# Optimization experiments

Hardware: AMD Instinct MI355X
Metric: run time of the kernel (lower is better)

Reference implementation:

```python
import jax, jax.numpy as jnp
import numpy as np

N, DIN, D, K0, NC = 32768, 768, 512, 128, 2
KS = [128, 64, 32, 16]  # prototype counts per stage (num_protos // 2**i)
NEG_SLOPE = 0.01


def _lin(x, W, b):
    # torch nn.Linear: W is [out, in]
    return x @ W.T + b


def _ln(x, g, b):
    m = x.mean(-1, keepdims=True)
    v = ((x - m) ** 2).mean(-1, keepdims=True)
    return (x - m) * jax.lax.rsqrt(v + 1e-5) * g + b


def setup_inputs() -> dict:
    key = jax.random.key(0)
    ks = jax.random.split(key, 40)
    s = 0.02

    def nrm(k, shp, sc=s):
        return jax.random.normal(k, shp, jnp.float32) * sc

    inp = {}
    inp["data"] = jax.random.normal(ks[0], (N, DIN), jnp.float32)
    inp["prototypes"] = jax.random.normal(ks[1], (K0, DIN), jnp.float32)
    inp["W_pp"] = nrm(ks[2], (D, DIN)); inp["b_pp"] = jnp.zeros((D,), jnp.float32)
    inp["W_cp"] = nrm(ks[3], (D, DIN)); inp["b_cp"] = jnp.zeros((D,), jnp.float32)
    inp["sim_scale"] = jnp.ones((1,), jnp.float32)
    # 3 enhancer MLPs + layernorms (stacked, same shapes)
    inp["enh_w1"] = nrm(ks[4], (3, D, D)); inp["enh_b1"] = jnp.zeros((3, D), jnp.float32)
    inp["enh_w2"] = nrm(ks[5], (3, D, D)); inp["enh_b2"] = jnp.zeros((3, D), jnp.float32)
    inp["ln_g"] = jnp.ones((3, D), jnp.float32); inp["ln_b"] = jnp.zeros((3, D), jnp.float32)
    # ProtoReducers: Mlp along K axis; fc1 [inK,inK], fc2 [outK,inK]
    ki = 6
    for i in range(3):
        inK, outK = KS[i], KS[i + 1]
        inp[f"red_w1_{i}"] = nrm(ks[ki], (inK, inK)); ki += 1
        inp[f"red_b1_{i}"] = jnp.zeros((inK,), jnp.float32)
        inp[f"red_w2_{i}"] = nrm(ks[ki], (outK, inK)); ki += 1
        inp[f"red_b2_{i}"] = jnp.zeros((outK,), jnp.float32)
    inp["W_proc"] = nrm(ks[20], (D, D)); inp["b_proc"] = jnp.zeros((D,), jnp.float32)
    inp["g_an"] = jnp.ones((D,), jnp.float32); inp["b_an"] = jnp.zeros((D,), jnp.float32)
    inp["W_t"] = nrm(ks[21], (D, D)); inp["b_t"] = jnp.zeros((D,), jnp.float32)
    inp["W_g"] = nrm(ks[22], (D, D)); inp["b_g"] = jnp.zeros((D,), jnp.float32)
    inp["W_s"] = nrm(ks[23], (1, D)); inp["b_s"] = jnp.zeros((1,), jnp.float32)
    inp["W_h"] = nrm(ks[24], (D, D)); inp["b_h"] = jnp.zeros((D,), jnp.float32)
    inp["W_c"] = nrm(ks[25], (NC, D)); inp["b_c"] = jnp.zeros((NC,), jnp.float32)
    return inp


def reference(data, prototypes, W_pp, b_pp, W_cp, b_cp, sim_scale,
              enh_w1, enh_b1, enh_w2, enh_b2, ln_g, ln_b,
              red_w1_0, red_b1_0, red_w2_0, red_b2_0,
              red_w1_1, red_b1_1, red_w2_1, red_b2_1,
              red_w1_2, red_b1_2, red_w2_2, red_b2_2,
              W_proc, b_proc, g_an, b_an,
              W_t, b_t, W_g, b_g, W_s, b_s, W_h, b_h, W_c, b_c):
    # patch / prototype projections (Linear + LeakyReLU)
    P = jax.nn.leaky_relu(_lin(data, W_pp, b_pp), NEG_SLOPE)        # [N, D]
    C = jax.nn.leaky_relu(_lin(prototypes, W_cp, b_cp), NEG_SLOPE)  # [K0, D]
    # denom = max(1e-6, tau * similarity_scale.item()); tau=1, no grad through scale
    denom = jnp.maximum(1e-6, jax.lax.stop_gradient(sim_scale)[0])
    reds = [(red_w1_0, red_b1_0, red_w2_0, red_b2_0),
            (red_w1_1, red_b1_1, red_w2_1, red_b2_1),
            (red_w1_2, red_b1_2, red_w2_2, red_b2_2)]
    for i in range(3):
        # L2 similarity: -cdist(P, C) computed as a GEMM
        d2 = (jnp.sum(P * P, -1, keepdims=True) + jnp.sum(C * C, -1)[None, :]
              - 2.0 * (P @ C.T))
        sim = -jnp.sqrt(jnp.maximum(d2, 1e-12))                     # [N, K]
        A = jax.nn.softmax(sim / denom, axis=1)                     # soft routing
        ctx = A @ C                                                 # [N, D]
        P = _ln(P + ctx, ln_g[i], ln_b[i])
        P = P + _lin(jax.nn.relu(_lin(P, enh_w1[i], enh_b1[i])), enh_w2[i], enh_b2[i])
        # ProtoReducer: Mlp over K axis (operate on C.T of shape [D, K])
        w1, b1, w2, b2 = reds[i]
        Ct = _lin(jax.nn.relu(_lin(C.T, w1, b1)), w2, b2)           # [D, Kout]
        C = Ct.T
    Z = jnp.concatenate([P, C], axis=0)                             # [N+16, D]
    Z = jax.nn.relu(_lin(Z, W_proc, b_proc))
    Z = _ln(Z, g_an, b_an)
    # gated attention MIL pooling
    t = jnp.tanh(_lin(Z, W_t, b_t))
    g = jax.nn.sigmoid(_lin(Z, W_g, b_g))
    scores = _lin(t * g, W_s, b_s)                                  # [N+16, 1]
    Aw = jax.nn.softmax(scores, axis=0)
    bag = Aw.T @ Z                                                  # [1, D]
    h = jax.nn.relu(_lin(bag, W_h, b_h))
    logits = _lin(h, W_c, b_c)                                      # [1, 2]
    return logits
```

## Files before the change

kernel.cpp:

```cpp
#include <hip/hip_runtime.h>
#include <math.h>

typedef _Float16 f16x8 __attribute__((ext_vector_type(8)));
typedef _Float16 f16x4 __attribute__((ext_vector_type(4)));
typedef float f32x4 __attribute__((ext_vector_type(4)));

#define TBM 256
#define TBN 128
#define TBK 32

#define AS1 __attribute__((address_space(1)))
#define AS3 __attribute__((address_space(3)))

__device__ __forceinline__ void gll16(const _Float16* g, _Float16* l)
{
    __builtin_amdgcn_global_load_lds((const AS1 unsigned int*)g,
                                     (AS3 unsigned int*)l, 16, 0, 0);
}

__device__ __forceinline__ int xcd_swz(int d, int nwg)
{
    int q = nwg >> 3, r = nwg & 7;
    int x = d & 7, idx = d >> 3;
    int base = x < r ? x * (q + 1) : r * (q + 1) + (x - r) * q;
    return base + idx;
}

__device__ __forceinline__ float fsigmoid(float x)
{
    return __builtin_amdgcn_rcpf(1.f + __expf(-x));
}
__device__ __forceinline__ float ftanh(float x)
{
    float ax = fabsf(x);
    float e = __expf(-2.f * ax);
    float t = (1.f - e) * __builtin_amdgcn_rcpf(1.f + e);
    return copysignf(t, x);
}

template<int ACT, bool F16OUT>
__global__ __launch_bounds__(256)
void dot_k(const float* __restrict__ X, const float* __restrict__ W,
           const float* __restrict__ bias, void* __restrict__ Yv,
           int M, int K)
{
    int gw = (blockIdx.x * 256 + threadIdx.x) >> 6;
    int lane = threadIdx.x & 63;
    if (gw >= M * 512) return;
    int r = gw >> 9, n = gw & 511;
    const float* xr = X + (size_t)r * K;
    const float* wr = W + (size_t)n * K;
    float d = 0.f;
    for (int t = 0; t < K; t += 256) {
        float4 a = *(const float4*)(xr + t + lane * 4);
        float4 b = *(const float4*)(wr + t + lane * 4);
        d += a.x * b.x + a.y * b.y + a.z * b.z + a.w * b.w;
    }
#pragma unroll
    for (int o = 32; o; o >>= 1) d += __shfl_xor(d, o);
    if (lane == 0) {
        float v = d + bias[n];
        if (ACT == 1) v = v > 0.f ? v : 0.01f * v;
        else if (ACT == 2) v = fmaxf(v, 0.f);
        if (F16OUT) ((_Float16*)Yv)[(size_t)r * 512 + n] = (_Float16)v;
        else        ((float*)Yv)[(size_t)r * 512 + n] = v;
    }
}

__global__ __launch_bounds__(256)
void cvtC2_k(const float* __restrict__ C, _Float16* __restrict__ Ch,
             _Float16* __restrict__ CTh, float* __restrict__ Csq, int Kin)
{
    int w = threadIdx.x >> 6, lane = threadIdx.x & 63;
    int row = blockIdx.x * 4 + w;
    if (row >= Kin) return;
    float4 a = *(const float4*)(C + (size_t)row * 512 + lane * 8);
    float4 b = *(const float4*)(C + (size_t)row * 512 + lane * 8 + 4);
    f16x8 h;
    h[0] = (_Float16)a.x; h[1] = (_Float16)a.y; h[2] = (_Float16)a.z; h[3] = (_Float16)a.w;
    h[4] = (_Float16)b.x; h[5] = (_Float16)b.y; h[6] = (_Float16)b.z; h[7] = (_Float16)b.w;
    *(f16x8*)(Ch + (size_t)row * 512 + lane * 8) = h;
    float s = 0.f;
#pragma unroll
    for (int q = 0; q < 8; q++) {
        float f = (float)h[q];
        s += f * f;
        CTh[(size_t)(lane * 8 + q) * Kin + row] = h[q];
    }
#pragma unroll
    for (int o = 32; o; o >>= 1) s += __shfl_xor(s, o);
    if (lane == 0) Csq[row] = s;
}

template<int MODE, int ACT, bool SQ>
__global__ __launch_bounds__(512)
void mgemm(const _Float16* __restrict__ A, const _Float16* __restrict__ B,
           const float* __restrict__ bias, _Float16* __restrict__ Yh,
           float* __restrict__ Psq, int M, int K, int Nout)
{
    __shared__ _Float16 As[2][TBM * TBK];
    __shared__ _Float16 Bs[2][TBN * TBK];
    const int tid = threadIdx.x;
    const int lane = tid & 63;
    const int wid = tid >> 6;
    const int wr = wid >> 1, wc = wid & 1;

    int bid = xcd_swz(blockIdx.y * gridDim.x + blockIdx.x, gridDim.x * gridDim.y);
    const int m0 = (bid / gridDim.x) * TBM;
    const int n0 = (bid % gridDim.x) * TBN;

    f32x4 acc[4][4] = {};
    const int nt = K / TBK;

    const int lrow = lane >> 2;
    const int lk = (lane & 3) * 8;

    auto stage = [&](int t, int buf) {
        const int k0 = t * TBK;
#pragma unroll
        for (int q = 0; q < 2; q++) {
            int c = wid * 2 + q;
            int r = c * 16 + lrow;
            int am = min(m0 + r, M - 1);
            gll16(A + (size_t)am * K + k0 + lk, &As[buf][c * 512]);
        }
        {
            int c = wid;
            int r = c * 16 + lrow;
            int bn = min(n0 + r, Nout - 1);
            gll16(B + (size_t)bn * K + k0 + lk, &Bs[buf][c * 512]);
        }
    };

    stage(0, 0);
    __syncthreads();
    for (int t = 0; t < nt; ++t) {
        const int cur = t & 1;
        if (t + 1 < nt) stage(t + 1, cur ^ 1);
        f16x8 af[4], bf[4];
#pragma unroll
        for (int mi = 0; mi < 4; mi++)
            af[mi] = *(const f16x8*)(&As[cur][(wr * 64 + mi * 16 + (lane & 15)) * TBK + (lane >> 4) * 8]);
#pragma unroll
        for (int nj = 0; nj < 4; nj++)
            bf[nj] = *(const f16x8*)(&Bs[cur][(wc * 64 + nj * 16 + (lane & 15)) * TBK + (lane >> 4) * 8]);
#pragma unroll
        for (int mi = 0; mi < 4; mi++)
#pragma unroll
            for (int nj = 0; nj < 4; nj++)
                acc[mi][nj] = __builtin_amdgcn_mfma_f32_16x16x32_f16(af[mi], bf[nj], acc[mi][nj], 0, 0, 0);
        __syncthreads();
    }

    _Float16* eb = &As[0][0];
    const int g = lane >> 4;
#pragma unroll
    for (int p = 0; p < 2; p++) {
        if (p) __syncthreads();
        if ((wr >> 1) == p) {
#pragma unroll
            for (int nj = 0; nj < 4; nj++) {
                int col = wc * 64 + nj * 16 + (lane & 15);
                float bv = bias ? bias[n0 + col] : 0.f;
#pragma unroll
                for (int mi = 0; mi < 4; mi++)
#pragma unroll
                    for (int r = 0; r < 4; r++) {
                        int lr = (wr & 1) * 64 + mi * 16 + g * 4 + r;
                        float v = acc[mi][nj][r] + bv;
                        if (MODE == 0) {
                            if (ACT == 1) v = v > 0.f ? v : 0.01f * v;
                            else if (ACT == 2) v = fmaxf(v, 0.f);
                        }
                        eb[lr * 128 + col] = (_Float16)v;
                    }
            }
        }
        __syncthreads();
        int t4 = tid * 4;
        int lr = t4 >> 4;
        int cbase = (t4 & 15) * 8;
        int m = m0 + p * 128 + lr;
        float sq = 0.f;
        if (m < M) {
#pragma unroll
            for (int q = 0; q < 4; q++) {
                int c0 = cbase + q * 8;
                f16x8 hv = *(f16x8*)(eb + lr * 128 + c0);
                size_t gidx = (size_t)m * Nout + n0 + c0;
                if (MODE == 1) {
                    f16x8 old = *(f16x8*)(Yh + gidx);
                    f16x8 nw;
#pragma unroll
                    for (int e = 0; e < 8; e++) {
                        float s = (float)old[e] + (float)hv[e];
                        nw[e] = (_Float16)s;
                    }
                    *(f16x8*)(Yh + gidx) = nw;
                    hv = nw;
                } else {
                    *(f16x8*)(Yh + gidx) = hv;
                }
                if (SQ) {
#pragma unroll
                    for (int e = 0; e < 8; e++) { float f = (float)hv[e]; sq += f * f; }
                }
            }
        }
        if (SQ) {
            sq += __shfl_xor(sq, 1);
            sq += __shfl_xor(sq, 2);
            if ((lane & 3) == 0 && m < M) atomicAdd(&Psq[m], sq);
        }
    }
}

__global__ __launch_bounds__(512)
void gatgemm(const _Float16* __restrict__ A, const _Float16* __restrict__ B1,
             const _Float16* __restrict__ B2, const float* __restrict__ c1,
             const float* __restrict__ c2, const float* __restrict__ Ws,
             float* __restrict__ scr, int M, int K, int Nout)
{
    __shared__ _Float16 As[2][TBM * TBK];
    __shared__ _Float16 B1s[2][TBN * TBK];
    __shared__ _Float16 B2s[2][TBN * TBK];
    const int tid = threadIdx.x;
    const int lane = tid & 63;
    const int wid = tid >> 6;
    const int wr = wid >> 1, wc = wid & 1;

    int bid = xcd_swz(blockIdx.y * gridDim.x + blockIdx.x, gridDim.x * gridDim.y);
    const int m0 = (bid / gridDim.x) * TBM;
    const int n0 = (bid % gridDim.x) * TBN;

    f32x4 acc1[4][4] = {};
    f32x4 acc2[4][4] = {};
    const int nt = K / TBK;

    const int lrow = lane >> 2;
    const int lk = (lane & 3) * 8;

    auto stage = [&](int t, int buf) {
        const int k0 = t * TBK;
#pragma unroll
        for (int q = 0; q < 2; q++) {
            int c = wid * 2 + q;
            int r = c * 16 + lrow;
            int am = min(m0 + r, M - 1);
            gll16(A + (size_t)am * K + k0 + lk, &As[buf][c * 512]);
        }
        {
            int c = wid;
            int r = c * 16 + lrow;
            int bn = min(n0 + r, Nout - 1);
            gll16(B1 + (size_t)bn * K + k0 + lk, &B1s[buf][c * 512]);
            gll16(B2 + (size_t)bn * K + k0 + lk, &B2s[buf][c * 512]);
        }
    };

    stage(0, 0);
    __syncthreads();
    for (int t = 0; t < nt; ++t) {
        const int cur = t & 1;
        if (t + 1 < nt) stage(t + 1, cur ^ 1);
        f16x8 af[4], bf1[4], bf2[4];
#pragma unroll
        for (int mi = 0; mi < 4; mi++)
            af[mi] = *(const f16x8*)(&As[cur][(wr * 64 + mi * 16 + (lane & 15)) * TBK + (lane >> 4) * 8]);
#pragma unroll
        for (int nj = 0; nj < 4; nj++) {
            int ro = (wc * 64 + nj * 16 + (lane & 15)) * TBK + (lane >> 4) * 8;
            bf1[nj] = *(const f16x8*)(&B1s[cur][ro]);
            bf2[nj] = *(const f16x8*)(&B2s[cur][ro]);
        }
#pragma unroll
        for (int mi = 0; mi < 4; mi++)
#pragma unroll
            for (int nj = 0; nj < 4; nj++) {
                acc1[mi][nj] = __builtin_amdgcn_mfma_f32_16x16x32_f16(af[mi], bf1[nj], acc1[mi][nj], 0, 0, 0);
                acc2[mi][nj] = __builtin_amdgcn_mfma_f32_16x16x32_f16(af[mi], bf2[nj], acc2[mi][nj], 0, 0, 0);
            }
        __syncthreads();
    }

    const int g = lane >> 4;
    float wsv[4];
#pragma unroll
    for (int nj = 0; nj < 4; nj++)
        wsv[nj] = Ws[n0 + wc * 64 + nj * 16 + (lane & 15)];
#pragma unroll
    for (int mi = 0; mi < 4; mi++) {
#pragma unroll
        for (int r = 0; r < 4; r++) {
            float p = 0.f;
#pragma unroll
            for (int nj = 0; nj < 4; nj++) {
                int col = n0 + wc * 64 + nj * 16 + (lane & 15);
                float t1 = ftanh(acc1[mi][nj][r] + c1[col]);
                float g1 = fsigmoid(acc2[mi][nj][r] + c2[col]);
                p += t1 * g1 * wsv[nj];
            }
#pragma unroll
            for (int o = 1; o < 16; o <<= 1) p += __shfl_xor(p, o);
            if ((lane & 15) == 0) {
                int m = m0 + wr * 64 + mi * 16 + g * 4 + r;
                if (m < M) atomicAdd(&scr[m], p);
            }
        }
    }
}

#define SBM 128
__global__ __launch_bounds__(256)
void simgemm(const _Float16* __restrict__ A, const _Float16* __restrict__ B,
             const float* __restrict__ Psq, const float* __restrict__ Csq,
             const float* __restrict__ sscale, _Float16* __restrict__ Ah,
             int M, int K, int Kin)
{
    __shared__ _Float16 As[2][SBM * TBK];
    __shared__ _Float16 Bs[2][SBM * TBK];
    __shared__ float redmx[2][SBM];
    __shared__ float redsm[2][SBM];
    const int tid = threadIdx.x;
    const int lane = tid & 63;
    const int wid = tid >> 6;
    const int wr = wid >> 1, wc = wid & 1;
    const int m0 = blockIdx.y * SBM;

    f32x4 acc[4][4] = {};
    const int nt = K / TBK;
    const int lrow = lane >> 2;
    const int lk = (lane & 3) * 8;

    auto stage = [&](int t, int buf) {
        const int k0 = t * TBK;
#pragma unroll
        for (int q = 0; q < 2; q++) {
            int c = wid * 2 + q;
            int r = c * 16 + lrow;
            int am = min(m0 + r, M - 1);
            int bn = min(r, Kin - 1);
            gll16(A + (size_t)am * K + k0 + lk, &As[buf][c * 512]);
            gll16(B + (size_t)bn * K + k0 + lk, &Bs[buf][c * 512]);
        }
    };

    stage(0, 0);
    __syncthreads();
    for (int t = 0; t < nt; ++t) {
        const int cur = t & 1;
        if (t + 1 < nt) stage(t + 1, cur ^ 1);
        f16x8 af[4], bf[4];
#pragma unroll
        for (int mi = 0; mi < 4; mi++)
            af[mi] = *(const f16x8*)(&As[cur][(wr * 64 + mi * 16 + (lane & 15)) * TBK + (lane >> 4) * 8]);
#pragma unroll
        for (int nj = 0; nj < 4; nj++)
            bf[nj] = *(const f16x8*)(&Bs[cur][(wc * 64 + nj * 16 + (lane & 15)) * TBK + (lane >> 4) * 8]);
#pragma unroll
        for (int mi = 0; mi < 4; mi++)
#pragma unroll
            for (int nj = 0; nj < 4; nj++)
                acc[mi][nj] = __builtin_amdgcn_mfma_f32_16x16x32_f16(af[mi], bf[nj], acc[mi][nj], 0, 0, 0);
        __syncthreads();
    }

    const float denom = fmaxf(1e-6f, sscale[0]);
    const int colbase = wc * 64 + (lane & 15);
    const int g = lane >> 4;
    float cc[4];
#pragma unroll
    for (int nj = 0; nj < 4; nj++) {
        int n = colbase + nj * 16;
        cc[nj] = (n < Kin) ? Csq[n] : 0.f;
    }

#pragma unroll
    for (int mi = 0; mi < 4; mi++) {
#pragma unroll
        for (int r = 0; r < 4; r++) {
            int row = wr * 64 + mi * 16 + g * 4 + r;
            float pp = Psq[m0 + row];
            float mx = -INFINITY;
#pragma unroll
            for (int nj = 0; nj < 4; nj++) {
                int n = colbase + nj * 16;
                float v = -INFINITY;
                if (n < Kin)
                    v = -sqrtf(fmaxf(pp + cc[nj] - 2.f * acc[mi][nj][r], 1e-12f)) / denom;
                acc[mi][nj][r] = v;
                mx = fmaxf(mx, v);
            }
#pragma unroll
            for (int o = 1; o < 16; o <<= 1) mx = fmaxf(mx, __shfl_xor(mx, o));
            if ((lane & 15) == 0) redmx[wc][row] = mx;
        }
    }
    __syncthreads();

#pragma unroll
    for (int mi = 0; mi < 4; mi++) {
#pragma unroll
        for (int r = 0; r < 4; r++) {
            int row = wr * 64 + mi * 16 + g * 4 + r;
            float mx = fmaxf(redmx[0][row], redmx[1][row]);
            float s = 0.f;
#pragma unroll
            for (int nj = 0; nj < 4; nj++) {
                int n = colbase + nj * 16;
                float e = (n < Kin) ? __expf(acc[mi][nj][r] - mx) : 0.f;
                acc[mi][nj][r] = e;
                s += e;
            }
#pragma unroll
            for (int o = 1; o < 16; o <<= 1) s += __shfl_xor(s, o);
            if ((lane & 15) == 0) redsm[wc][row] = s;
        }
    }
    __syncthreads();

#pragma unroll
    for (int mi = 0; mi < 4; mi++) {
#pragma unroll
        for (int r = 0; r < 4; r++) {
            int row = wr * 64 + mi * 16 + g * 4 + r;
            float inv = __builtin_amdgcn_rcpf(redsm[0][row] + redsm[1][row]);
            int m = m0 + row;
#pragma unroll
            for (int nj = 0; nj < 4; nj++) {
                int n = colbase + nj * 16;
                if (n < Kin)
                    Ah[(size_t)m * Kin + n] = (_Float16)(acc[mi][nj][r] * inv);
            }
        }
    }
}

__global__ __launch_bounds__(256)
void cvt_k(const float* __restrict__ x, _Float16* __restrict__ y, int n)
{
    int i = (blockIdx.x * 256 + threadIdx.x) * 4;
    if (i < n) {
        float4 v = *(const float4*)(x + i);
        f16x4 h = { (_Float16)v.x, (_Float16)v.y, (_Float16)v.z, (_Float16)v.w };
        *(f16x4*)(y + i) = h;
    }
}

__global__ __launch_bounds__(256)
void ln_k(const _Float16* __restrict__ X, const _Float16* __restrict__ R,
          const float* __restrict__ g, const float* __restrict__ b,
          _Float16* __restrict__ Yh, int M)
{
    int wid = threadIdx.x >> 6, lane = threadIdx.x & 63;
    int row = blockIdx.x * 4 + wid;
    if (row >= M) return;
    f16x8 a = *(const f16x8*)(X + (size_t)row * 512 + lane * 8);
    float v[8];
#pragma unroll
    for (int q = 0; q < 8; q++) v[q] = (float)a[q];
    if (R) {
        f16x8 c = *(const f16x8*)(R + (size_t)row * 512 + lane * 8);
#pragma unroll
        for (int q = 0; q < 8; q++) v[q] += (float)c[q];
    }
    float s = 0.f, ss = 0.f;
#pragma unroll
    for (int q = 0; q < 8; q++) { s += v[q]; ss += v[q] * v[q]; }
#pragma unroll
    for (int o = 32; o; o >>= 1) { s += __shfl_xor(s, o); ss += __shfl_xor(ss, o); }
    float mean = s * (1.f / 512.f);
    float var = ss * (1.f / 512.f) - mean * mean;
    float inv = 1.f / sqrtf(var + 1e-5f);
    int d0 = lane * 8;
    f16x8 o8;
#pragma unroll
    for (int q = 0; q < 8; q++)
        o8[q] = (_Float16)((v[q] - mean) * inv * g[d0 + q] + b[d0 + q]);
    *(f16x8*)(Yh + (size_t)row * 512 + d0) = o8;
}

__global__ __launch_bounds__(256)
void red1_k(const float* __restrict__ C, const float* __restrict__ w1,
            const float* __restrict__ b1, float* __restrict__ H1, int Kin)
{
    int d = blockIdx.x * 256 + threadIdx.x;
    int j = blockIdx.y;
    float acc = b1[j];
    for (int k = 0; k < Kin; k++) acc = fmaf(C[(size_t)k * 512 + d], w1[(size_t)j * Kin + k], acc);
    H1[(size_t)j * 512 + d] = fmaxf(acc, 0.f);
}

__global__ __launch_bounds__(256)
void red2_k(const float* __restrict__ H1, const float* __restrict__ w2,
            const float* __restrict__ b2, float* __restrict__ Cn,
            _Float16* __restrict__ Chn, _Float16* __restrict__ CThn,
            float* __restrict__ Csqn, int Kin, int Kout)
{
    int d = blockIdx.x * 256 + threadIdx.x;
    int j2 = blockIdx.y;
    float acc = b2[j2];
    for (int j = 0; j < Kin; j++) acc = fmaf(H1[(size_t)j * 512 + d], w2[(size_t)j2 * Kin + j], acc);
    Cn[(size_t)j2 * 512 + d] = acc;
    _Float16 h = (_Float16)acc;
    Chn[(size_t)j2 * 512 + d] = h;
    CThn[(size_t)d * Kout + j2] = h;
    float f = (float)h;
    float sq = f * f;
#pragma unroll
    for (int o = 32; o; o >>= 1) sq += __shfl_xor(sq, o);
    if ((threadIdx.x & 63) == 0) atomicAdd(&Csqn[j2], sq);
}

__global__ __launch_bounds__(1024)
void pool_k(float* __restrict__ s, float* __restrict__ scal, int M)
{
    __shared__ float sm[16];
    int tid = threadIdx.x, lane = tid & 63, wid = tid >> 6;
    float mx = -INFINITY;
    for (int i = tid * 4; i < M; i += 4096) {
        float4 a = *(const float4*)(s + i);
        mx = fmaxf(fmaxf(fmaxf(mx, a.x), fmaxf(a.y, a.z)), a.w);
    }
#pragma unroll
    for (int o = 32; o; o >>= 1) mx = fmaxf(mx, __shfl_xor(mx, o));
    if (lane == 0) sm[wid] = mx;
    __syncthreads();
    if (wid == 0) {
        float v = (lane < 16) ? sm[lane] : -INFINITY;
#pragma unroll
        for (int o = 8; o; o >>= 1) v = fmaxf(v, __shfl_xor(v, o));
        if (lane == 0) sm[0] = v;
    }
    __syncthreads();
    float gmax = sm[0];
    __syncthreads();
    float sum = 0.f;
    for (int i = tid * 4; i < M; i += 4096) {
        float4 a = *(const float4*)(s + i);
        float4 e;
        e.x = __expf(a.x - gmax); e.y = __expf(a.y - gmax);
        e.z = __expf(a.z - gmax); e.w = __expf(a.w - gmax);
        *(float4*)(s + i) = e;
        sum += e.x + e.y + e.z + e.w;
    }
#pragma unroll
    for (int o = 32; o; o >>= 1) sum += __shfl_xor(sum, o);
    if (lane == 0) sm[wid] = sum;
    __syncthreads();
    if (tid == 0) {
        float t = 0.f;
        for (int w = 0; w < 16; w++) t += sm[w];
        scal[0] = t;
    }
}

__global__ __launch_bounds__(256)
void bagp_k(const _Float16* __restrict__ Z, const float* __restrict__ w,
            float* __restrict__ PB, int M, int cs)
{
    int d = blockIdx.x * 256 + threadIdx.x;
    int chunk = blockIdx.y;
    int i0 = chunk * cs;
    int i1 = min(M, i0 + cs);
    float acc = 0.f;
    for (int i = i0; i < i1; i++) acc = fmaf(w[i], (float)Z[(size_t)i * 512 + d], acc);
    PB[(size_t)chunk * 512 + d] = acc;
}

__global__ __launch_bounds__(256)
void bagf_k(const float* __restrict__ PB, const float* __restrict__ scal,
            float* __restrict__ bag, int nchunk)
{
    int d = blockIdx.x * 256 + threadIdx.x;
    float acc = 0.f;
    for (int c = 0; c < nchunk; c++) acc += PB[(size_t)c * 512 + d];
    bag[d] = acc / scal[0];
}

__global__ __launch_bounds__(256)
void h_k(const float* __restrict__ bag, const float* __restrict__ Wh,
         const float* __restrict__ bh, float* __restrict__ h)
{
    int wid = threadIdx.x >> 6, lane = threadIdx.x & 63;
    int j = blockIdx.x * 4 + wid;
    const float* wr = Wh + (size_t)j * 512;
    float d = 0.f;
#pragma unroll
    for (int t = 0; t < 2; t++) {
        float4 a = *(const float4*)(wr + t * 256 + lane * 4);
        float4 bv = *(const float4*)(bag + t * 256 + lane * 4);
        d += a.x * bv.x + a.y * bv.y + a.z * bv.z + a.w * bv.w;
    }
#pragma unroll
    for (int o = 32; o; o >>= 1) d += __shfl_xor(d, o);
    if (lane == 0) h[j] = fmaxf(d + bh[j], 0.f);
}

__global__ __launch_bounds__(128)
void logit_k(const float* __restrict__ h, const float* __restrict__ Wc,
             const float* __restrict__ bc, float* __restrict__ out)
{
    int wid = threadIdx.x >> 6, lane = threadIdx.x & 63;
    const float* wr = Wc + (size_t)wid * 512;
    float d = 0.f;
#pragma unroll
    for (int t = 0; t < 2; t++) {
        float4 a = *(const float4*)(wr + t * 256 + lane * 4);
        float4 hv = *(const float4*)(h + t * 256 + lane * 4);
        d += a.x * hv.x + a.y * hv.y + a.z * hv.z + a.w * hv.w;
    }
#pragma unroll
    for (int o = 32; o; o >>= 1) d += __shfl_xor(d, o);
    if (lane == 0) out[wid] = d + bc[wid];
}

extern "C" void kernel_launch(void* const* d_in, const int* in_sizes, int n_in,
                              void* d_out, int out_size, void* d_ws, size_t ws_size,
                              hipStream_t stream)
{
    const float* data    = (const float*)d_in[0];
    const float* protos  = (const float*)d_in[1];
    const float* W_pp    = (const float*)d_in[2];
    const float* b_pp    = (const float*)d_in[3];
    const float* W_cp    = (const float*)d_in[4];
    const float* b_cp    = (const float*)d_in[5];
    const float* sscale  = (const float*)d_in[6];
    const float* enh_w1  = (const float*)d_in[7];
    const float* enh_b1  = (const float*)d_in[8];
    const float* enh_w2  = (const float*)d_in[9];
    const float* enh_b2  = (const float*)d_in[10];
    const float* ln_g    = (const float*)d_in[11];
    const float* ln_b    = (const float*)d_in[12];
    const float* red_w1[3] = {(const float*)d_in[13], (const float*)d_in[17], (const float*)d_in[21]};
    const float* red_b1[3] = {(const float*)d_in[14], (const float*)d_in[18], (const float*)d_in[22]};
    const float* red_w2[3] = {(const float*)d_in[15], (const float*)d_in[19], (const float*)d_in[23]};
    const float* red_b2[3] = {(const float*)d_in[16], (const float*)d_in[20], (const float*)d_in[24]};
    const float* W_proc  = (const float*)d_in[25];
    const float* b_proc  = (const float*)d_in[26];
    const float* g_an    = (const float*)d_in[27];
    const float* b_an    = (const float*)d_in[28];
    const float* W_t     = (const float*)d_in[29];
    const float* b_t     = (const float*)d_in[30];
    const float* W_g     = (const float*)d_in[31];
    const float* b_g     = (const float*)d_in[32];
    const float* W_s     = (const float*)d_in[33];
    const float* b_s     = (const float*)d_in[34];
    const float* W_h     = (const float*)d_in[35];
    const float* b_h     = (const float*)d_in[36];
    const float* W_c     = (const float*)d_in[37];
    const float* b_c     = (const float*)d_in[38];
    float* out = (float*)d_out;
    (void)b_s;

    constexpr int N = 32768, DIN = 768, D = 512;
    constexpr int NCHUNK = 256;
    char* w = (char*)d_ws;
    auto alloc = [&](size_t bytes) -> char* {
        char* p = w; w += (bytes + 255) & ~(size_t)255; return p;
    };
    _Float16* Ph     = (_Float16*)alloc((size_t)N * D * 2);
    _Float16* CTXh   = (_Float16*)alloc((size_t)N * D * 2);
    _Float16* TMPh   = (_Float16*)alloc((size_t)N * D * 2);
    _Float16* Zrawh  = (_Float16*)alloc((size_t)(N + 16) * D * 2);
    _Float16* Zh     = (_Float16*)alloc((size_t)(N + 16) * D * 2);
    _Float16* datah  = (_Float16*)alloc((size_t)N * DIN * 2);
    _Float16* Ah     = (_Float16*)alloc((size_t)N * 128 * 2);
    _Float16* Ch     = (_Float16*)alloc(128 * D * 2);
    _Float16* CTh    = (_Float16*)alloc(128 * D * 2);
    _Float16* Wpph   = (_Float16*)alloc((size_t)D * DIN * 2);
    _Float16* w1h    = (_Float16*)alloc((size_t)3 * D * D * 2);
    _Float16* w2h    = (_Float16*)alloc((size_t)3 * D * D * 2);
    _Float16* Wproch = (_Float16*)alloc((size_t)D * D * 2);
    _Float16* Wth    = (_Float16*)alloc((size_t)D * D * 2);
    _Float16* Wgh    = (_Float16*)alloc((size_t)D * D * 2);
    float*    Psq    = (float*)alloc((size_t)N * 4);
    float*    Csq    = (float*)alloc(128 * 4);
    float*    Ca     = (float*)alloc(128 * D * 4);
    float*    Cb     = (float*)alloc(128 * D * 4);
    float*    H1     = (float*)alloc(128 * D * 4);
    float*    scr    = (float*)alloc((size_t)(N + 16) * 4);
    float*    PB     = (float*)alloc((size_t)NCHUNK * D * 4);
    float*    bag    = (float*)alloc(D * 4);
    float*    hb     = (float*)alloc(D * 4);
    float*    scal   = (float*)alloc(8 * 4);

    dim3 blk(256);
    dim3 blk512(512);
    auto cgrid = [](size_t n) { return dim3((unsigned)((n / 4 + 255) / 256)); };
    auto mgrid = [](int M_, int Nout_) { return dim3((Nout_ + TBN - 1) / TBN, (M_ + TBM - 1) / TBM); };

    cvt_k<<<cgrid((size_t)N * DIN), blk, 0, stream>>>(data, datah, N * DIN);
    cvt_k<<<cgrid((size_t)D * DIN), blk, 0, stream>>>(W_pp, Wpph, D * DIN);
    cvt_k<<<cgrid((size_t)3 * D * D), blk, 0, stream>>>(enh_w1, w1h, 3 * D * D);
    cvt_k<<<cgrid((size_t)3 * D * D), blk, 0, stream>>>(enh_w2, w2h, 3 * D * D);
    cvt_k<<<cgrid((size_t)D * D), blk, 0, stream>>>(W_proc, Wproch, D * D);
    cvt_k<<<cgrid((size_t)D * D), blk, 0, stream>>>(W_t, Wth, D * D);
    cvt_k<<<cgrid((size_t)D * D), blk, 0, stream>>>(W_g, Wgh, D * D);

    hipMemsetAsync(Psq, 0, (size_t)N * 4, stream);
    mgemm<0, 1, true><<<mgrid(N, D), blk512, 0, stream>>>(datah, Wpph, b_pp, Ph, Psq, N, DIN, D);
    dot_k<1, false><<<dim3(128 * 512 / 4), blk, 0, stream>>>(protos, W_cp, b_cp, Ca, 128, DIN);
    cvtC2_k<<<dim3(32), blk, 0, stream>>>(Ca, Ch, CTh, Csq, 128);

    float* C = Ca;
    float* Cn = Cb;
    int Kin = 128;
    for (int i = 0; i < 3; i++) {
        int Kout = Kin >> 1;
        simgemm<<<dim3(1, N / SBM), blk, 0, stream>>>(Ph, Ch, Psq, Csq, sscale, Ah, N, D, Kin);
        if (i < 2) hipMemsetAsync(Psq, 0, (size_t)N * 4, stream);
        mgemm<0, 0, false><<<mgrid(N, D), blk512, 0, stream>>>(Ah, CTh, nullptr, CTXh, nullptr, N, Kin, D);
        ln_k<<<dim3((N + 3) / 4), blk, 0, stream>>>(Ph, CTXh, ln_g + (size_t)i * D, ln_b + (size_t)i * D, Ph, N);
        mgemm<0, 2, false><<<mgrid(N, D), blk512, 0, stream>>>(Ph, w1h + (size_t)i * D * D, enh_b1 + (size_t)i * D, TMPh, nullptr, N, D, D);
        if (i < 2)
            mgemm<1, 0, true><<<mgrid(N, D), blk512, 0, stream>>>(TMPh, w2h + (size_t)i * D * D, enh_b2 + (size_t)i * D, Ph, Psq, N, D, D);
        else
            mgemm<1, 0, false><<<mgrid(N, D), blk512, 0, stream>>>(TMPh, w2h + (size_t)i * D * D, enh_b2 + (size_t)i * D, Ph, nullptr, N, D, D);
        hipMemsetAsync(Csq, 0, 128 * 4, stream);
        red1_k<<<dim3(2, Kin), blk, 0, stream>>>(C, red_w1[i], red_b1[i], H1, Kin);
        red2_k<<<dim3(2, Kout), blk, 0, stream>>>(H1, red_w2[i], red_b2[i], Cn, Ch, CTh, Csq, Kin, Kout);
        float* t = C; C = Cn; Cn = t;
        Kin = Kout;
    }

    mgemm<0, 2, false><<<mgrid(N, D), blk512, 0, stream>>>(Ph, Wproch, b_proc, Zrawh, nullptr, N, D, D);
    dot_k<2, true><<<dim3(16 * 512 / 4), blk, 0, stream>>>(C, W_proc, b_proc, Zrawh + (size_t)N * D, 16, D);
    ln_k<<<dim3((N + 16 + 3) / 4), blk, 0, stream>>>(Zrawh, nullptr, g_an, b_an, Zh, N + 16);

    hipMemsetAsync(scr, 0, (size_t)(N + 16) * 4, stream);
    gatgemm<<<mgrid(N + 16, D), blk512, 0, stream>>>(Zh, Wth, Wgh, b_t, b_g, W_s, scr, N + 16, D, D);

    pool_k<<<dim3(1), dim3(1024), 0, stream>>>(scr, scal, N + 16);
    int cs = (N + 16 + NCHUNK - 1) / NCHUNK;
    bagp_k<<<dim3(2, NCHUNK), blk, 0, stream>>>(Zh, scr, PB, N + 16, cs);
    bagf_k<<<dim3(2), blk, 0, stream>>>(PB, scal, bag, NCHUNK);

    h_k<<<dim3(128), blk, 0, stream>>>(bag, W_h, b_h, hb);
    logit_k<<<dim3(1), dim3(128), 0, stream>>>(hb, W_c, b_c, out);
}
```

Measured before the change: 858.0 us.

## Fuse context GEMM (A@C) with residual add and LayerNorm into one kernel

Replaces the separate ctx GEMM plus LayerNorm kernel with a single kernel. Each block computes a full 128x512 row tile of A@C, stages it in shared memory, and applies the residual add and LayerNorm in place on Ph. This removes the CTX buffer round trip through global memory and one launch per stage. In exchange each block covers all 512 columns, giving a larger accumulator footprint per thread and only 256 blocks, which may lower occupancy and parallelism.

```diff
diff --git a/kernel.cpp b/kernel.cpp
--- a/kernel.cpp
+++ b/kernel.cpp
@@ -211,6 +211,106 @@
             sq += __shfl_xor(sq, 1);
             sq += __shfl_xor(sq, 2);
             if ((lane & 3) == 0 && m < M) atomicAdd(&Psq[m], sq);
+        }
+    }
+}
+
+__global__ __launch_bounds__(512)
+void ctxln_k(const _Float16* __restrict__ A, const _Float16* __restrict__ CT,
+             const float* __restrict__ g, const float* __restrict__ b,
+             _Float16* __restrict__ Ph, int M, int Kin)
+{
+    __shared__ _Float16 As[2][128 * TBK];
+    __shared__ _Float16 Bs[2][512 * TBK];
+    const int tid = threadIdx.x;
+    const int lane = tid & 63;
+    const int wid = tid >> 6;
+    const int wr = wid >> 2, wc = wid & 3;
+    const int m0 = blockIdx.y * 128;
+
+    f32x4 acc[4][8] = {};
+    const int nt = Kin / TBK;
+
+    const int lrow = lane >> 2;
+    const int lk = (lane & 3) * 8;
+
+    auto stage = [&](int t, int buf) {
+        const int k0 = t * TBK;
+        {
+            int r = wid * 16 + lrow;
+            gll16(A + (size_t)(m0 + r) * Kin + k0 + lk, &As[buf][wid * 512]);
+        }
+#pragma unroll
+        for (int q = 0; q < 4; q++) {
+            int c = wid * 4 + q;
+            int n = c * 16 + lrow;
+            gll16(CT + (size_t)n * Kin + k0 + lk, &Bs[buf][c * 512]);
+        }
+    };
+
+    stage(0, 0);
+    __syncthreads();
+    for (int t = 0; t < nt; ++t) {
+        const int cur = t & 1;
+        if (t + 1 < nt) stage(t + 1, cur ^ 1);
+        f16x8 af[4], bf[8];
+#pragma unroll
+        for (int mi = 0; mi < 4; mi++)
+            af[mi] = *(const f16x8*)(&As[cur][(wr * 64 + mi * 16 + (lane & 15)) * TBK + (lane >> 4) * 8]);
+#pragma unroll
+        for (int nj = 0; nj < 8; nj++)
+            bf[nj] = *(const f16x8*)(&Bs[cur][(wc * 128 + nj * 16 + (lane & 15)) * TBK + (lane >> 4) * 8]);
+#pragma unroll
+        for (int mi = 0; mi < 4; mi++)
+#pragma unroll
+            for (int nj = 0; nj < 8; nj++)
+                acc[mi][nj] = __builtin_amdgcn_mfma_f32_16x16x32_f16(af[mi], bf[nj], acc[mi][nj], 0, 0, 0);
+        __syncthreads();
+    }
+
+    _Float16* eb = &Bs[0][0];
+    const int gq = lane >> 4;
+#pragma unroll
+    for (int p = 0; p < 2; p++) {
+        if (p) __syncthreads();
+        if (wr == p) {
+#pragma unroll
+            for (int nj = 0; nj < 8; nj++) {
+                int col = wc * 128 + nj * 16 + (lane & 15);
+#pragma unroll
+                for (int mi = 0; mi < 4; mi++)
+#pragma unroll
+                    for (int r = 0; r < 4; r++) {
+                        int lr = mi * 16 + gq * 4 + r;
+                        eb[lr * 512 + col] = (_Float16)acc[mi][nj][r];
+                    }
+            }
+        }
+        __syncthreads();
+#pragma unroll
+        for (int rr = 0; rr < 8; rr++) {
+            int lr = wid * 8 + rr;
+            int m = m0 + p * 64 + lr;
+            f16x8 cv = *(f16x8*)(eb + lr * 512 + lane * 8);
+            f16x8 pv = *(const f16x8*)(Ph + (size_t)m * 512 + lane * 8);
+            float v[8];
+            float s = 0.f, ss = 0.f;
+#pragma unroll
+            for (int q = 0; q < 8; q++) {
+                v[q] = (float)pv[q] + (float)cv[q];
+                s += v[q]; ss += v[q] * v[q];
+            }
+#pragma unroll
+            for (int o = 32; o; o >>= 1) { s += __shfl_xor(s, o); ss += __shfl_xor(ss, o); }
+            float mean = s * (1.f / 512.f);
+            float var = ss * (1.f / 512.f) - mean * mean;
+            float inv = 1.f / sqrtf(var + 1e-5f);
+            int d0 = lane * 8;
+            f16x8 o8;
+#pragma unroll
+            for (int q = 0; q < 8; q++)
+                o8[q] = (_Float16)((v[q] - mean) * inv * g[d0 + q] + b[d0 + q]);
+            *(f16x8*)(Ph + (size_t)m * 512 + d0) = o8;
         }
     }
 }
@@ -660,7 +760,6 @@
         char* p = w; w += (bytes + 255) & ~(size_t)255; return p;
     };
     _Float16* Ph     = (_Float16*)alloc((size_t)N * D * 2);
-    _Float16* CTXh   = (_Float16*)alloc((size_t)N * D * 2);
     _Float16* TMPh   = (_Float16*)alloc((size_t)N * D * 2);
     _Float16* Zrawh  = (_Float16*)alloc((size_t)(N + 16) * D * 2);
     _Float16* Zh     = (_Float16*)alloc((size_t)(N + 16) * D * 2);
@@ -710,8 +809,7 @@
         int Kout = Kin >> 1;
         simgemm<<<dim3(1, N / SBM), blk, 0, stream>>>(Ph, Ch, Psq, Csq, sscale, Ah, N, D, Kin);
         if (i < 2) hipMemsetAsync(Psq, 0, (size_t)N * 4, stream);
-        mgemm<0, 0, false><<<mgrid(N, D), blk512, 0, stream>>>(Ah, CTh, nullptr, CTXh, nullptr, N, Kin, D);
-        ln_k<<<dim3((N + 3) / 4), blk, 0, stream>>>(Ph, CTXh, ln_g + (size_t)i * D, ln_b + (size_t)i * D, Ph, N);
+        ctxln_k<<<dim3(1, N / 128), blk512, 0, stream>>>(Ah, CTh, ln_g + (size_t)i * D, ln_b + (size_t)i * D, Ph, N, Kin);
         mgemm<0, 2, false><<<mgrid(N, D), blk512, 0, stream>>>(Ph, w1h + (size_t)i * D * D, enh_b1 + (size_t)i * D, TMPh, nullptr, N, D, D);
         if (i < 2)
             mgemm<1, 0, true><<<mgrid(N, D), blk512, 0, stream>>>(TMPh, w2h + (size_t)i * D * D, enh_b2 + (size_t)i * D, Ph, Psq, N, D, D);
```

Result: faster. 813.8 us (-5.2%).
